# Kernel optimization log

Hardware: AMD Instinct MI355X
Metric: run time of the kernel (lower is better)

Reference implementation:

```python
import jax, jax.numpy as jnp
import numpy as np


def setup_inputs() -> dict:
    key = jax.random.key(0)
    feats = jax.random.normal(key, (16, 64, 128, 128), dtype=jnp.float32)
    return {"feats": feats, "stride": 2}


def reference(feats, stride):
    # Zero-insertion upsampling: equivalent to conv_transpose2d with an
    # s x s kernel whose only nonzero is at [0,0], stride=s, groups=C.
    # out[b,c,i*s,j*s] = feats[b,c,i,j]; all other entries are zero.
    B, C, H, W = feats.shape
    out = jnp.zeros((B, C, H * stride, W * stride), dtype=feats.dtype)
    out = out.at[:, :, ::stride, ::stride].set(feats)
    return out
```

## Files before the change

kernel.cpp:

```cpp
#include <hip/hip_runtime.h>


#define IN_W   128
#define PAIRS  (16 * 64 * 128)

typedef float f2 __attribute__((ext_vector_type(2)));
typedef float f4 __attribute__((ext_vector_type(4)));

__global__ __launch_bounds__(256) void pad_within_kernel(
    const float* __restrict__ in, float* __restrict__ out) {
    const unsigned lane = threadIdx.x & 63u;
    const unsigned wid  = (blockIdx.x * blockDim.x + threadIdx.x) >> 6;
    const unsigned nw   = (gridDim.x * blockDim.x) >> 6;

    const f4 zero = {0.f, 0.f, 0.f, 0.f};

    #pragma unroll 4
    for (unsigned p = wid; p < PAIRS; p += nw) {
        const f2* irow = (const f2*)(in + (size_t)p * IN_W);
        f2 x = __builtin_nontemporal_load(&irow[lane]);

        f4 val = {x.x, 0.f, x.y, 0.f};

        f4* opair = (f4*)(out + (size_t)p * 512);
        __builtin_nontemporal_store(val,  &opair[lane]);
        __builtin_nontemporal_store(zero, &opair[64u + lane]);
    }
}

extern "C" void kernel_launch(void* const* d_in, const int* in_sizes, int n_in,
                              void* d_out, int out_size, void* d_ws, size_t ws_size,
                              hipStream_t stream) {
    const float* feats = (const float*)d_in[0];
    float* out = (float*)d_out;
    dim3 block(256);
    dim3 grid(2048);
    pad_within_kernel<<<grid, block, 0, stream>>>(feats, out);
}
```

Baseline: 309.5 us.

## Split into full-buffer zero fill kernel plus scatter of input values

Replaces the single fused kernel with two launches. The first zeroes the whole output with vec4 stores, and the second rewrites the even rows with interleaved input values. This simplifies each kernel and drops the grid-stride loop and nontemporal hints. In exchange, the even output rows are written twice and there is an extra launch, which adds roughly a quarter more write traffic.

```diff
diff --git a/kernel.cpp b/kernel.cpp
--- a/kernel.cpp
+++ b/kernel.cpp
@@ -1,31 +1,22 @@
 #include <hip/hip_runtime.h>
 
-
-#define IN_W   128
-#define PAIRS  (16 * 64 * 128)
 
 typedef float f2 __attribute__((ext_vector_type(2)));
 typedef float f4 __attribute__((ext_vector_type(4)));
 
-__global__ __launch_bounds__(256) void pad_within_kernel(
+__global__ __launch_bounds__(256) void zero_kernel(float* __restrict__ out) {
+    unsigned v = blockIdx.x * blockDim.x + threadIdx.x;
+    ((f4*)out)[v] = (f4){0.f, 0.f, 0.f, 0.f};
+}
+
+__global__ __launch_bounds__(256) void scatter_kernel(
     const float* __restrict__ in, float* __restrict__ out) {
-    const unsigned lane = threadIdx.x & 63u;
-    const unsigned wid  = (blockIdx.x * blockDim.x + threadIdx.x) >> 6;
-    const unsigned nw   = (gridDim.x * blockDim.x) >> 6;
-
-    const f4 zero = {0.f, 0.f, 0.f, 0.f};
-
-    #pragma unroll 4
-    for (unsigned p = wid; p < PAIRS; p += nw) {
-        const f2* irow = (const f2*)(in + (size_t)p * IN_W);
-        f2 x = __builtin_nontemporal_load(&irow[lane]);
-
-        f4 val = {x.x, 0.f, x.y, 0.f};
-
-        f4* opair = (f4*)(out + (size_t)p * 512);
-        __builtin_nontemporal_store(val,  &opair[lane]);
-        __builtin_nontemporal_store(zero, &opair[64u + lane]);
-    }
+    unsigned v = blockIdx.x * blockDim.x + threadIdx.x;
+    unsigned t = v & 63u;
+    unsigned p = v >> 6;
+    f2 x = ((const f2*)in)[v];
+    f4* dst = (f4*)(out + (size_t)p * 512 + (size_t)t * 4);
+    *dst = (f4){x.x, 0.f, x.y, 0.f};
 }
 
 extern "C" void kernel_launch(void* const* d_in, const int* in_sizes, int n_in,
@@ -33,7 +24,8 @@
                               hipStream_t stream) {
     const float* feats = (const float*)d_in[0];
     float* out = (float*)d_out;
-    dim3 block(256);
-    dim3 grid(2048);
-    pad_within_kernel<<<grid, block, 0, stream>>>(feats, out);
+    unsigned n_vec4 = (unsigned)(out_size / 4);
+    zero_kernel<<<dim3(n_vec4 / 256), dim3(256), 0, stream>>>(out);
+    unsigned n_f2 = 8388608u;
+    scatter_kernel<<<dim3(n_f2 / 256), dim3(256), 0, stream>>>(feats, out);
 }
```

Result: no change. 313.8 us (+1.4%).
